# Optimization experiments

Hardware: AMD Instinct MI355X
Metric: run time of the kernel (lower is better)

The kernel has to match this reference:

```python
import jax, jax.numpy as jnp
import numpy as np

DIM = 1024
N_HEADS = 16
HEAD_DIM = DIM // N_HEADS
COND_DIM = 1024
MLP_RATIO = 4
B = 8
L = 1024  # per-sequence length (equal lengths -> T = B*L packed tokens)
T = B * L
EPS = 1e-5


def setup_inputs() -> dict:
    key = jax.random.key(0)
    ks = jax.random.split(key, 16)
    s = 0.02
    # rotary tables: [max_pos, head_dim//2]
    inv_freq = 1.0 / (10000.0 ** (jnp.arange(0, HEAD_DIM, 2, dtype=jnp.float32) / HEAD_DIM))
    t = jnp.arange(L, dtype=jnp.float32)
    freqs = t[:, None] * inv_freq[None, :]  # [L, HEAD_DIM//2]
    return {
        "x": jax.random.normal(ks[0], (T, DIM), jnp.float32),
        "lengths": jnp.full((B,), L, dtype=jnp.int64),
        "offsets": jnp.arange(B, dtype=jnp.int64) * L,
        "cos": jnp.cos(freqs),
        "sin": jnp.sin(freqs),
        "positions": jnp.tile(jnp.arange(L, dtype=jnp.int64), B),
        "c": jax.random.normal(ks[1], (B, COND_DIM), jnp.float32),
        "ln1_w": jnp.ones((DIM,), jnp.float32),
        "Wq": jax.random.normal(ks[2], (DIM, DIM), jnp.float32) * s,
        "Wk": jax.random.normal(ks[3], (DIM, DIM), jnp.float32) * s,
        "Wv": jax.random.normal(ks[4], (DIM, DIM), jnp.float32) * s,
        "Wo": jax.random.normal(ks[5], (DIM, DIM), jnp.float32) * s,
        "ln2_w": jnp.ones((DIM,), jnp.float32),
        "W1": jax.random.normal(ks[6], (DIM, MLP_RATIO * DIM), jnp.float32) * s,
        "b1": jnp.zeros((MLP_RATIO * DIM,), jnp.float32),
        "W2": jax.random.normal(ks[7], (MLP_RATIO * DIM, DIM), jnp.float32) * s,
        "b2": jnp.zeros((DIM,), jnp.float32),
        "ada_w": jax.random.normal(ks[8], (COND_DIM, 6 * DIM), jnp.float32) * s,
        "ada_b": jnp.zeros((6 * DIM,), jnp.float32),
    }


def _layer_norm(x, w):
    # LayerNorm with weight only (no bias), as in the torch module
    mu = jnp.mean(x, axis=-1, keepdims=True)
    var = jnp.mean(jnp.square(x - mu), axis=-1, keepdims=True)
    return (x - mu) * jax.lax.rsqrt(var + EPS) * w


def _rope(q, k, cos, sin, positions):
    # q, k: [T, H, D]; cos/sin: [max_pos, D//2]; half-split RoPE
    c = cos[positions][:, None, :]  # [T, 1, D//2]
    s = sin[positions][:, None, :]
    def rot(x):
        x1, x2 = jnp.split(x, 2, axis=-1)
        return jnp.concatenate([x1 * c - x2 * s, x2 * c + x1 * s], axis=-1)
    return rot(q), rot(k)


def reference(x, lengths, offsets, cos, sin, positions, c,
              ln1_w, Wq, Wk, Wv, Wo, ln2_w, W1, b1, W2, b2, ada_w, ada_b):
    # adaLN modulation: [B, 6*DIM] -> six [B, DIM]
    ada = c @ ada_w + ada_b
    sh_msa, sc_msa, g_msa, sh_mlp, sc_mlp, g_mlp = jnp.split(ada, 6, axis=-1)
    # per-token gather via seq_ids (equal lengths -> repeat each row L times)
    seq_ids = jnp.repeat(jnp.arange(B), L)  # = repeat_interleave(arange(B), lengths)
    sh_msa_t, sc_msa_t, g_msa_t = sh_msa[seq_ids], sc_msa[seq_ids], g_msa[seq_ids]
    sh_mlp_t, sc_mlp_t, g_mlp_t = sh_mlp[seq_ids], sc_mlp[seq_ids], g_mlp[seq_ids]

    x_skip = x
    h = _layer_norm(x, ln1_w) * (1.0 + sc_msa_t) + sh_msa_t
    q = (h @ Wq).reshape(T, N_HEADS, HEAD_DIM)
    k = (h @ Wk).reshape(T, N_HEADS, HEAD_DIM)
    v = (h @ Wv).reshape(T, N_HEADS, HEAD_DIM)
    q, k = _rope(q, k, cos, sin, positions)

    # intra-sequence-only attention: with equal lengths the block-diagonal
    # score_mod mask is exactly per-sequence attention -> reshape to [B, L, H, D]
    qb = q.reshape(B, L, N_HEADS, HEAD_DIM)
    kb = k.reshape(B, L, N_HEADS, HEAD_DIM)
    vb = v.reshape(B, L, N_HEADS, HEAD_DIM)
    scores = jnp.einsum('blhd,bmhd->bhlm', qb, kb) / jnp.sqrt(jnp.float32(HEAD_DIM))
    probs = jax.nn.softmax(scores, axis=-1)
    attn = jnp.einsum('bhlm,bmhd->blhd', probs, vb).reshape(T, DIM)

    x = x_skip + g_msa_t * (attn @ Wo)  # dropout p is identity in eval mode

    h2 = _layer_norm(x, ln2_w) * (1.0 + sc_mlp_t) + sh_mlp_t
    mlp = jax.nn.gelu(h2 @ W1 + b1, approximate=True) @ W2 + b2
    return x + g_mlp_t * mlp
```

## Files before the change

kernel.cpp:

```cpp
#include <hip/hip_runtime.h>

typedef unsigned short u16;
typedef __attribute__((ext_vector_type(8))) short short8;
typedef __attribute__((ext_vector_type(4))) float f32x4;
typedef __attribute__((ext_vector_type(4))) unsigned uint4v;

__device__ __forceinline__ float bf2f(u16 u){
  unsigned v = ((unsigned)u) << 16;
  return __builtin_bit_cast(float, v);
}
__device__ __forceinline__ u16 f2bf(float f){
  unsigned u = __builtin_bit_cast(unsigned, f);
  u += 0x7fff + ((u >> 16) & 1);
  return (u16)(u >> 16);
}
__device__ __forceinline__ unsigned packbf(float lo, float hi){
  return ((unsigned)f2bf(hi) << 16) | (unsigned)f2bf(lo);
}
__device__ __forceinline__ void async16(const void* g, void* l){
  __builtin_amdgcn_global_load_lds((const __attribute__((address_space(1))) void*)g,
                                   (__attribute__((address_space(3))) void*)l, 16, 0, 0);
}
#define VMW(n) asm volatile("s_waitcnt vmcnt(" #n ")" ::: "memory")

__global__ __launch_bounds__(256) void ada_partial(
    const float* __restrict__ c, const float* __restrict__ aw,
    float* __restrict__ part){
  int n  = blockIdx.x*256 + threadIdx.x;
  int b  = blockIdx.y;
  int kc = blockIdx.z;
  const float* cr  = c + b*1024 + kc*128;
  const float* awp = aw + (size_t)(kc*128)*6144 + n;
  float acc = 0.f;
#pragma unroll 8
  for (int k = 0; k < 128; ++k)
    acc += cr[k] * awp[(size_t)k*6144];
  part[(size_t)(kc*8 + b)*6144 + n] = acc;
}

__global__ __launch_bounds__(256) void ada_reduce(
    const float* __restrict__ part, const float* __restrict__ ab,
    float* __restrict__ ada){
  int idx = blockIdx.x*256 + threadIdx.x;
  int n = idx % 6144;
  float acc = ab[n];
#pragma unroll
  for (int kc = 0; kc < 8; ++kc)
    acc += part[(size_t)kc*49152 + idx];
  ada[idx] = acc;
}

__global__ __launch_bounds__(256) void transpose_cast(
    const float* __restrict__ src, u16* __restrict__ dst, int K, int N){
  __shared__ float t[64][65];
  int n0 = blockIdx.x*64, k0 = blockIdx.y*64;
  int tid = threadIdx.x;
  int cc = tid & 63, r4 = tid >> 6;
#pragma unroll 4
  for (int it = 0; it < 16; ++it){
    int r = it*4 + r4;
    t[r][cc] = src[(size_t)(k0 + r)*N + n0 + cc];
  }
  __syncthreads();
#pragma unroll 4
  for (int it = 0; it < 16; ++it){
    int r = it*4 + r4;
    dst[(size_t)(n0 + r)*K + k0 + cc] = f2bf(t[cc][r]);
  }
}

__global__ __launch_bounds__(256) void ln_mod(
    const float* __restrict__ x, u16* __restrict__ out,
    const float* __restrict__ w, const float* __restrict__ ada,
    int shift_off, int scale_off){
  int t = blockIdx.x, tid = threadIdx.x;
  const float* xr = x + (size_t)t*1024;
  float v[4]; float s = 0.f, ss = 0.f;
#pragma unroll
  for (int i = 0; i < 4; ++i){ v[i] = xr[tid + i*256]; s += v[i]; ss += v[i]*v[i]; }
  for (int d = 1; d < 64; d <<= 1){ s += __shfl_xor(s, d); ss += __shfl_xor(ss, d); }
  __shared__ float red[8];
  int wv = tid >> 6;
  if ((tid & 63) == 0){ red[wv] = s; red[4+wv] = ss; }
  __syncthreads();
  s = red[0]+red[1]+red[2]+red[3];
  ss = red[4]+red[5]+red[6]+red[7];
  float mu = s * (1.f/1024.f);
  float var = ss * (1.f/1024.f) - mu*mu;
  float rs = rsqrtf(var + 1e-5f);
  int b = t >> 10;
  const float* sh = ada + b*6144 + shift_off;
  const float* sc = ada + b*6144 + scale_off;
#pragma unroll
  for (int i = 0; i < 4; ++i){
    int cidx = tid + i*256;
    float hh = (v[i]-mu)*rs*w[cidx]*(1.f + sc[cidx]) + sh[cidx];
    out[(size_t)t*1024 + cidx] = f2bf(hh);
  }
}

template<int EPI>
__device__ __forceinline__ void gemm_epi(
    void* Cout, int m, int n, int N, int m_off, float v,
    const float* e0, const float* e1, const float* e2){
  if (EPI == 0){
    ((u16*)Cout)[(size_t)m*N + n] = f2bf(v);
  } else if (EPI == 1){
    const int b = (m + m_off) >> 10;
    float g = e1[b*6144 + 2048 + n];
    ((float*)Cout)[(size_t)m*N + n] = e0[(size_t)m*N + n] + g*v;
  } else if (EPI == 2){
    float xx = v + e0[n];
    float u = xx*(1.5957691216f + 0.07135481626f*xx*xx);
    ((u16*)Cout)[(size_t)m*N + n] = f2bf(xx / (1.f + __expf(-u)));
  } else {
    const int b = (m + m_off) >> 10;
    float g = e1[b*6144 + 5120 + n];
    ((float*)Cout)[(size_t)m*N + n] = e2[(size_t)m*N + n] + g*(v + e0[n]);
  }
}

__device__ __forceinline__ void xcd_remap(int& bx, int& by){
  const int nx = gridDim.x;
  const int yb = gridDim.y >> 3;
  const int bid = blockIdx.y*nx + blockIdx.x;
  const int g = bid & 7, ii = bid >> 3;
  bx = ii % nx;
  by = g*yb + ii/nx;
}

template<int EPI>
__global__ __launch_bounds__(512, 2) void gemm_bt(
    const u16* __restrict__ A, const u16* __restrict__ Bt,
    void* __restrict__ Cout, int M, int N, int K, int m_off,
    const float* __restrict__ e0, const float* __restrict__ e1,
    const float* __restrict__ e2){
  __shared__ u16 lds[32768];
  const int tid = threadIdx.x;
  const int wv = tid >> 6, lane = tid & 63;
  const int quad = lane >> 4, ln = lane & 15;
  const int wr = wv >> 2, wc = wv & 3;
  int bx, by; xcd_remap(bx, by);
  const int n0 = bx*256, m0 = by*256;
  const int nt = K >> 5;

  const int swslot = (lane & 3) ^ ((lane >> 3) & 3);
  const u16* Ap = A  + (size_t)(m0 + wv*16 + (lane>>2))*K + swslot*8;
  const u16* Bp = Bt + (size_t)(n0 + wv*16 + (lane>>2))*K + swslot*8;
  const size_t hstep = (size_t)128*K;
  u16* lw = lds + wv*512;

  f32x4 acc[8][4] = {};

  async16(Ap,         lw);
  async16(Ap + hstep, lw + 4096);
  async16(Bp,         lw + 8192);
  async16(Bp + hstep, lw + 12288);
  VMW(0);
  __builtin_amdgcn_s_barrier();

  const int rsw = (quad ^ ((ln >> 1) & 3))*8;
  const u16* Ar = lds + (wr*128 + ln)*32 + rsw;
  const u16* Br = lds + 8192 + (wc*64 + ln)*32 + rsw;

  for (int t = 0; t < nt; ++t){
    const int bo = (t & 1)*16384;
    short8 bfr[4], af[4];
#pragma unroll
    for (int j = 0; j < 4; ++j) bfr[j] = *(const short8*)(Br + bo + j*512);
#pragma unroll
    for (int i = 0; i < 4; ++i) af[i]  = *(const short8*)(Ar + bo + i*512);
    if (t + 1 < nt){
      u16* d = lw + ((t+1)&1)*16384;
      async16(Ap + (size_t)(t+1)*32,         d);
      async16(Ap + hstep + (size_t)(t+1)*32, d + 4096);
      async16(Bp + (size_t)(t+1)*32,         d + 8192);
      async16(Bp + hstep + (size_t)(t+1)*32, d + 12288);
    }
    __builtin_amdgcn_s_setprio(1);
#pragma unroll
    for (int i = 0; i < 4; ++i)
#pragma unroll
      for (int j = 0; j < 4; ++j)
        acc[i][j] = __builtin_amdgcn_mfma_f32_16x16x32_bf16(af[i], bfr[j], acc[i][j], 0, 0, 0);
#pragma unroll
    for (int i = 0; i < 4; ++i) af[i] = *(const short8*)(Ar + bo + 2048 + i*512);
#pragma unroll
    for (int i = 0; i < 4; ++i)
#pragma unroll
      for (int j = 0; j < 4; ++j)
        acc[4+i][j] = __builtin_amdgcn_mfma_f32_16x16x32_bf16(af[i], bfr[j], acc[4+i][j], 0, 0, 0);
    __builtin_amdgcn_s_setprio(0);
    VMW(0);
    __builtin_amdgcn_s_barrier();
  }

  const int mB = m0 + wr*128 + quad*4;
  const int nB = n0 + wc*64 + ln;
#pragma unroll
  for (int i = 0; i < 8; ++i)
#pragma unroll
    for (int r = 0; r < 4; ++r)
#pragma unroll
      for (int j = 0; j < 4; ++j)
        gemm_epi<EPI>(Cout, mB + i*16 + r, nB + j*16, N, m_off, acc[i][j][r], e0, e1, e2);
}

template<int EPI>
__global__ __launch_bounds__(256, 4) void gemm_bt128(
    const u16* __restrict__ A, const u16* __restrict__ Bt,
    void* __restrict__ Cout, int M, int N, int K, int m_off,
    const float* __restrict__ e0, const float* __restrict__ e1,
    const float* __restrict__ e2){
  __shared__ u16 lds[32768];
  const int tid = threadIdx.x;
  const int wv = tid >> 6, lane = tid & 63;
  const int quad = lane >> 4, ln = lane & 15;
  const int wr = wv >> 1, wc = wv & 1;
  int bx, by; xcd_remap(bx, by);
  const int n0 = bx*128, m0 = by*128;
  const int nt = K >> 5;

  const int swslot = (lane & 3) ^ ((lane >> 3) & 3);
  const u16* Ap = A  + (size_t)(m0 + wv*16 + (lane>>2))*K + swslot*8;
  const u16* Bp = Bt + (size_t)(n0 + wv*16 + (lane>>2))*K + swslot*8;
  const size_t hstep = (size_t)64*K;
  u16* lw = lds + wv*512;

  f32x4 acc[4][4] = {};

#pragma unroll
  for (int tau = 0; tau < 3; ++tau){
    u16* d = lw + tau*8192;
    async16(Ap + (size_t)tau*32,         d);
    async16(Ap + hstep + (size_t)tau*32, d + 2048);
    async16(Bp + (size_t)tau*32,         d + 4096);
    async16(Bp + hstep + (size_t)tau*32, d + 6144);
  }
  VMW(8);
  __builtin_amdgcn_s_barrier();

  const int rsw = (quad ^ ((ln >> 1) & 3))*8;
  const u16* Ar = lds + (wr*64 + ln)*32 + rsw;
  const u16* Br = lds + 4096 + (wc*64 + ln)*32 + rsw;

  for (int t = 0; t < nt; ++t){
    const int bo = (t & 3)*8192;
    short8 bfr[4], af[2];
#pragma unroll
    for (int j = 0; j < 4; ++j) bfr[j] = *(const short8*)(Br + bo + j*512);
#pragma unroll
    for (int i = 0; i < 2; ++i) af[i]  = *(const short8*)(Ar + bo + i*512);
    if (t + 3 < nt){
      u16* d = lw + ((t+3)&3)*8192;
      async16(Ap + (size_t)(t+3)*32,         d);
      async16(Ap + hstep + (size_t)(t+3)*32, d + 2048);
      async16(Bp + (size_t)(t+3)*32,         d + 4096);
      async16(Bp + hstep + (size_t)(t+3)*32, d + 6144);
    }
    __builtin_amdgcn_s_setprio(1);
#pragma unroll
    for (int i = 0; i < 2; ++i)
#pragma unroll
      for (int j = 0; j < 4; ++j)
        acc[i][j] = __builtin_amdgcn_mfma_f32_16x16x32_bf16(af[i], bfr[j], acc[i][j], 0, 0, 0);
#pragma unroll
    for (int i = 0; i < 2; ++i) af[i] = *(const short8*)(Ar + bo + 1024 + i*512);
#pragma unroll
    for (int i = 0; i < 2; ++i)
#pragma unroll
      for (int j = 0; j < 4; ++j)
        acc[2+i][j] = __builtin_amdgcn_mfma_f32_16x16x32_bf16(af[i], bfr[j], acc[2+i][j], 0, 0, 0);
    __builtin_amdgcn_s_setprio(0);
    if (t + 4 <= nt)      VMW(8);
    else if (t + 3 == nt) VMW(4);
    else if (t + 2 == nt) VMW(0);
    __builtin_amdgcn_s_barrier();
  }

  const int mB = m0 + wr*64 + quad*4;
  const int nB = n0 + wc*64 + ln;
#pragma unroll
  for (int i = 0; i < 4; ++i)
#pragma unroll
    for (int r = 0; r < 4; ++r)
#pragma unroll
      for (int j = 0; j < 4; ++j)
        gemm_epi<EPI>(Cout, mB + i*16 + r, nB + j*16, N, m_off, acc[i][j][r], e0, e1, e2);
}

__global__ __launch_bounds__(256) void rope_pack(
    const u16* __restrict__ qkv, const float* __restrict__ cosT,
    const float* __restrict__ sinT, u16* __restrict__ qp,
    u16* __restrict__ kp, u16* __restrict__ vt){
  int blk = blockIdx.x;
  int lt = blk & 15, h = (blk >> 4) & 15, b = blk >> 8;
  int l0 = lt*64;
  int bh = b*16 + h;
  __shared__ u16 vl[64][68];
  int tid = threadIdx.x;
  size_t tile_base = (size_t)bh*65536 + (size_t)lt*4096;
#pragma unroll 4
  for (int it = 0; it < 16; ++it){
    int idx = it*256 + tid;
    int r = idx >> 6, d = idx & 63;
    int t = b*1024 + l0 + r;
    int pos = l0 + r;
    const u16* row = qkv + (size_t)t*3072 + h*64;
    float qv = bf2f(row[d]), kv = bf2f(row[1024+d]);
    float qo, ko;
    if (d < 32){
      float cs = cosT[pos*32 + d], sn = sinT[pos*32 + d];
      qo = qv*cs - bf2f(row[d+32])*sn;
      ko = kv*cs - bf2f(row[1024+d+32])*sn;
    } else {
      int dd = d - 32;
      float cs = cosT[pos*32 + dd], sn = sinT[pos*32 + dd];
      qo = qv*cs + bf2f(row[d-32])*sn;
      ko = kv*cs + bf2f(row[1024+d-32])*sn;
    }
    qp[((size_t)bh*1024 + l0 + r)*64 + d] = f2bf(qo*0.125f);
    int ksl = ((d&31) >> 3) ^ ((r >> 1) & 3);
    kp[tile_base + (d>>5)*2048 + r*32 + (ksl<<3) + (d&7)] = f2bf(ko);
    vl[d][r] = row[2048 + d];
  }
  __syncthreads();
#pragma unroll 4
  for (int it = 0; it < 16; ++it){
    int idx = it*256 + tid;
    int d = idx >> 6, cc = idx & 63;
    int vsl = ((cc&31) >> 3) ^ ((d >> 1) & 3);
    vt[tile_base + (cc>>5)*2048 + d*32 + (vsl<<3) + (cc&7)] = vl[d][cc];
  }
}

__global__ __launch_bounds__(256) void attn_kernel(
    const u16* __restrict__ qp, const u16* __restrict__ kp,
    const u16* __restrict__ vtp, u16* __restrict__ ao){
  __shared__ u16 Kb[2][4096];
  __shared__ u16 Vb[2][4096];
  int tid = threadIdx.x, w = tid >> 6, lane = tid & 63;
  int quad = lane >> 4, ln = lane & 15;
  int bh = blockIdx.x & 127, qb = blockIdx.x >> 7;
  int h = bh & 15, b = bh >> 4;
  const u16* Q  = qp  + ((size_t)bh*1024 + qb*64 + w*16)*64;
  const u16* Kg = kp  + (size_t)bh*65536 + lane*8;
  const u16* Vg = vtp + (size_t)bh*65536 + lane*8;
  short8 qf0 = *(const short8*)(Q + ln*64 + quad*8);
  short8 qf1 = *(const short8*)(Q + ln*64 + 32 + quad*8);
  f32x4 o[4] = {};
  float m = -3e38f, l = 0.f;
  const int rsw = (quad ^ ((ln >> 1) & 3))*8;

  async16(Kg + (w*2+0)*512, Kb[0] + (w*2+0)*512);
  async16(Kg + (w*2+1)*512, Kb[0] + (w*2+1)*512);
  async16(Vg + (w*2+0)*512, Vb[0] + (w*2+0)*512);
  async16(Vg + (w*2+1)*512, Vb[0] + (w*2+1)*512);

  for (int kt = 0; kt < 16; ++kt){
    const int cur = kt & 1;
    if (kt < 15){
      const u16* ktg = Kg + (kt+1)*4096;
      const u16* vtg = Vg + (kt+1)*4096;
      async16(ktg + (w*2+0)*512, Kb[cur^1] + (w*2+0)*512);
      async16(ktg + (w*2+1)*512, Kb[cur^1] + (w*2+1)*512);
      async16(vtg + (w*2+0)*512, Vb[cur^1] + (w*2+0)*512);
      async16(vtg + (w*2+1)*512, Vb[cur^1] + (w*2+1)*512);
      VMW(4);
    } else {
      VMW(0);
    }
    __builtin_amdgcn_s_barrier();
    f32x4 zz = {0.f, 0.f, 0.f, 0.f};
    f32x4 st[4];
    __builtin_amdgcn_s_setprio(1);
#pragma unroll
    for (int c = 0; c < 4; ++c){
      short8 k0 = *(const short8*)(Kb[cur] +        (c*16 + ln)*32 + rsw);
      short8 k1 = *(const short8*)(Kb[cur] + 2048 + (c*16 + ln)*32 + rsw);
      st[c] = __builtin_amdgcn_mfma_f32_16x16x32_bf16(k0, qf0, zz, 0,0,0);
      st[c] = __builtin_amdgcn_mfma_f32_16x16x32_bf16(k1, qf1, st[c], 0,0,0);
    }
    __builtin_amdgcn_s_setprio(0);
    short8 va[4][2];
#pragma unroll
    for (int dc = 0; dc < 4; ++dc)
#pragma unroll
      for (int kh = 0; kh < 2; ++kh)
        va[dc][kh] = *(const short8*)(Vb[cur] + kh*2048 + (dc*16 + ln)*32 + rsw);
    float mx = st[0][0];
#pragma unroll
    for (int c = 0; c < 4; ++c)
#pragma unroll
      for (int r = 0; r < 4; ++r) mx = fmaxf(mx, st[c][r]);
    mx = fmaxf(mx, __shfl_xor(mx, 16));
    mx = fmaxf(mx, __shfl_xor(mx, 32));
    if (__any(mx > m + 8.f)){
      float mn = fmaxf(m, mx);
      float alpha = __expf(m - mn);
      m = mn;
      l *= alpha;
#pragma unroll
      for (int dc = 0; dc < 4; ++dc)
#pragma unroll
        for (int r = 0; r < 4; ++r) o[dc][r] *= alpha;
    }
    float p[4][4];
#pragma unroll
    for (int c = 0; c < 4; ++c)
#pragma unroll
      for (int r = 0; r < 4; ++r) p[c][r] = __expf(st[c][r] - m);
    float sum = ((p[0][0]+p[0][1]) + (p[0][2]+p[0][3])) + ((p[1][0]+p[1][1]) + (p[1][2]+p[1][3]))
              + ((p[2][0]+p[2][1]) + (p[2][2]+p[2][3])) + ((p[3][0]+p[3][1]) + (p[3][2]+p[3][3]));
    sum += __shfl_xor(sum, 16);
    sum += __shfl_xor(sum, 32);
    l += sum;
    unsigned pc[4][2];
#pragma unroll
    for (int c = 0; c < 4; ++c){
      pc[c][0] = packbf(p[c][0], p[c][1]);
      pc[c][1] = packbf(p[c][2], p[c][3]);
    }
    const int sA = ((quad & 1)*2)*16 + ln;
    const int sB = sA + 16;
    const bool hi = quad >= 2;
#pragma unroll
    for (int kh = 0; kh < 2; ++kh){
      unsigned a0 = (unsigned)__shfl((int)pc[2*kh][0],   sA);
      unsigned b0 = (unsigned)__shfl((int)pc[2*kh+1][0], sA);
      unsigned a1 = (unsigned)__shfl((int)pc[2*kh][1],   sA);
      unsigned b1 = (unsigned)__shfl((int)pc[2*kh+1][1], sA);
      unsigned a2 = (unsigned)__shfl((int)pc[2*kh][0],   sB);
      unsigned b2 = (unsigned)__shfl((int)pc[2*kh+1][0], sB);
      unsigned a3 = (unsigned)__shfl((int)pc[2*kh][1],   sB);
      unsigned b3 = (unsigned)__shfl((int)pc[2*kh+1][1], sB);
      uint4v u = { hi ? b0 : a0, hi ? b1 : a1, hi ? b2 : a2, hi ? b3 : a3 };
      short8 pfrag = __builtin_bit_cast(short8, u);
      __builtin_amdgcn_s_setprio(1);
#pragma unroll
      for (int dc = 0; dc < 4; ++dc)
        o[dc] = __builtin_amdgcn_mfma_f32_16x16x32_bf16(va[dc][kh], pfrag, o[dc], 0,0,0);
      __builtin_amdgcn_s_setprio(0);
    }
    __builtin_amdgcn_s_barrier();
  }
  float rl = 1.f / l;
  size_t orow = ((size_t)b*1024 + qb*64 + w*16 + ln)*1024 + h*64;
#pragma unroll
  for (int dc = 0; dc < 4; ++dc)
#pragma unroll
    for (int r = 0; r < 4; ++r)
      ao[orow + dc*16 + quad*4 + r] = f2bf(o[dc][r] * rl);
}

extern "C" void kernel_launch(void* const* d_in, const int* in_sizes, int n_in,
                              void* d_out, int out_size, void* d_ws, size_t ws_size,
                              hipStream_t stream){
  const float* x    = (const float*)d_in[0];
  const float* cosT = (const float*)d_in[3];
  const float* sinT = (const float*)d_in[4];
  const float* c    = (const float*)d_in[6];
  const float* ln1w = (const float*)d_in[7];
  const float* Wq   = (const float*)d_in[8];
  const float* Wk   = (const float*)d_in[9];
  const float* Wv   = (const float*)d_in[10];
  const float* Wo   = (const float*)d_in[11];
  const float* ln2w = (const float*)d_in[12];
  const float* W1   = (const float*)d_in[13];
  const float* b1   = (const float*)d_in[14];
  const float* W2   = (const float*)d_in[15];
  const float* b2   = (const float*)d_in[16];
  const float* adaW = (const float*)d_in[17];
  const float* adaB = (const float*)d_in[18];

  char* ws = (char*)d_ws;
  float* ada  = (float*)(ws);
  u16* wqkvt  = (u16*)  (ws + 262144);
  u16* wot    = (u16*)  (ws + 6553600);
  u16* w1t    = (u16*)  (ws + 8650752);
  u16* w2t    = (u16*)  (ws + 17039360);
  u16* h      = (u16*)  (ws + 25427968);
  u16* qp     = (u16*)  (ws + 25427968);
  u16* h2     = (u16*)  (ws + 25427968);
  u16* qkv    = (u16*)  (ws + 42205184);
  u16* attnb  = (u16*)  (ws + 42205184);
  float* xmid = (float*)(ws + 58982400);
  float* adaP = (float*)(ws + 92536832);
  u16* kp     = (u16*)  (ws + 92536832);
  u16* vt     = (u16*)  (ws + 109314048);
  u16* hid    = (u16*)  (ws + 92536832);
  u16* hidF   = (u16*)  (ws + 126091264);
  float* out  = (float*)d_out;
  const bool bigws = ws_size >= (size_t)193200128;

  ada_partial<<<dim3(24,8,8), 256, 0, stream>>>(c, adaW, adaP);
  ada_reduce<<<192, 256, 0, stream>>>(adaP, adaB, ada);
  transpose_cast<<<dim3(16,16), 256, 0, stream>>>(Wq, wqkvt,             1024, 1024);
  transpose_cast<<<dim3(16,16), 256, 0, stream>>>(Wk, wqkvt + 1024*1024, 1024, 1024);
  transpose_cast<<<dim3(16,16), 256, 0, stream>>>(Wv, wqkvt + 2048*1024, 1024, 1024);
  transpose_cast<<<dim3(16,16), 256, 0, stream>>>(Wo, wot,               1024, 1024);
  transpose_cast<<<dim3(64,16), 256, 0, stream>>>(W1, w1t,               1024, 4096);
  transpose_cast<<<dim3(16,64), 256, 0, stream>>>(W2, w2t,               4096, 1024);
  ln_mod<<<8192, 256, 0, stream>>>(x, h, ln1w, ada, 0, 1024);
  gemm_bt128<0><<<dim3(24,64), 256, 0, stream>>>(h, wqkvt, qkv, 8192, 3072, 1024, 0,
                                                 nullptr, nullptr, nullptr);
  rope_pack<<<2048, 256, 0, stream>>>(qkv, cosT, sinT, qp, kp, vt);
  attn_kernel<<<2048, 256, 0, stream>>>(qp, kp, vt, attnb);
  gemm_bt128<1><<<dim3(8,64), 256, 0, stream>>>(attnb, wot, xmid, 8192, 1024, 1024, 0,
                                                x, ada, nullptr);
  ln_mod<<<8192, 256, 0, stream>>>(xmid, h2, ln2w, ada, 3072, 4096);
  if (bigws){
    gemm_bt<2><<<dim3(16,32), 512, 0, stream>>>(h2, w1t, hidF, 8192, 4096, 1024, 0,
                                                b1, nullptr, nullptr);
    gemm_bt128<3><<<dim3(8,64), 256, 0, stream>>>(hidF, w2t, out, 8192, 1024, 4096, 0,
                                                  b2, ada, xmid);
  } else {
    for (int cch = 0; cch < 2; ++cch){
      const size_t mo = (size_t)cch*4096;
      gemm_bt<2><<<dim3(16,16), 512, 0, stream>>>(h2 + mo*1024, w1t, hid,
                                                  4096, 4096, 1024, (int)mo,
                                                  b1, nullptr, nullptr);
      gemm_bt128<3><<<dim3(8,32), 256, 0, stream>>>(hid, w2t, out + mo*1024,
                                                    4096, 1024, 4096, (int)mo,
                                                    b2, ada, xmid + mo*1024);
    }
  }
}
```

Before: 581.8 us.

## Restructure 256x256 GEMM into 8-phase K=64 double-buffered pipeline

The 256x256 bf16 GEMM moves from a K=32 double-buffered loop to K=64 tiles in a 128KB LDS double buffer, with a new 8-way XOR swizzle. Each iteration handles two tiles in eight phases that interleave LDS fragment reads, partial async global-to-LDS loads and 16-MFMA bursts, separated by barriers and staged vmcnt waits. The goal is to hide global load latency behind MFMA work and cut per-K-step overhead. In exchange it uses twice the LDS per block, which likely allows only one 512-thread block per CU despite the launch bounds of 2, and it adds many barriers.

Result: slower. 608.8 us (+4.6%).

```diff
diff --git a/kernel.cpp b/kernel.cpp
--- a/kernel.cpp
+++ b/kernel.cpp
@@ -22,6 +22,7 @@
                                    (__attribute__((address_space(3))) void*)l, 16, 0, 0);
 }
 #define VMW(n) asm volatile("s_waitcnt vmcnt(" #n ")" ::: "memory")
+#define BARR() __builtin_amdgcn_s_barrier()
 
 __global__ __launch_bounds__(256) void ada_partial(
     const float* __restrict__ c, const float* __restrict__ aw,
@@ -129,71 +130,149 @@
   by = g*yb + ii/nx;
 }
 
+__device__ __forceinline__ void mfma16(f32x4 (&acc)[8][4], const short8 (&af)[4],
+                                       const short8 (&bf)[4], int ro){
+#pragma unroll
+  for (int i = 0; i < 4; ++i)
+#pragma unroll
+    for (int j = 0; j < 4; ++j)
+      acc[ro+i][j] = __builtin_amdgcn_mfma_f32_16x16x32_bf16(af[i], bf[j], acc[ro+i][j], 0,0,0);
+}
+__device__ __forceinline__ void ld4(short8 (&f)[4], const u16* base){
+#pragma unroll
+  for (int i = 0; i < 4; ++i) f[i] = *(const short8*)(base + i*1024);
+}
+
 template<int EPI>
 __global__ __launch_bounds__(512, 2) void gemm_bt(
     const u16* __restrict__ A, const u16* __restrict__ Bt,
     void* __restrict__ Cout, int M, int N, int K, int m_off,
     const float* __restrict__ e0, const float* __restrict__ e1,
     const float* __restrict__ e2){
-  __shared__ u16 lds[32768];
+  __shared__ u16 lds[65536];
   const int tid = threadIdx.x;
   const int wv = tid >> 6, lane = tid & 63;
   const int quad = lane >> 4, ln = lane & 15;
   const int wr = wv >> 2, wc = wv & 3;
   int bx, by; xcd_remap(bx, by);
   const int n0 = bx*256, m0 = by*256;
-  const int nt = K >> 5;
-
-  const int swslot = (lane & 3) ^ ((lane >> 3) & 3);
-  const u16* Ap = A  + (size_t)(m0 + wv*16 + (lane>>2))*K + swslot*8;
-  const u16* Bp = Bt + (size_t)(n0 + wv*16 + (lane>>2))*K + swslot*8;
-  const size_t hstep = (size_t)128*K;
-  u16* lw = lds + wv*512;
+  const int nIt = K >> 7;
+
+  const int srow  = wv*8 + (lane>>3);
+  const int sslot = (lane&7) ^ ((lane>>3)&7);
+  const u16* ApS = A  + (size_t)(m0 + srow)*K + sslot*8;
+  const u16* BpS = Bt + (size_t)(n0 + srow)*K + sslot*8;
+  const size_t qstep = (size_t)64*K;
+
+#define STA(s, T, buf) async16(ApS + (size_t)(s)*qstep + (size_t)(T)*64, \
+                               lds + (buf)*32768 + (s)*4096 + wv*512 + lane*8)
+#define STB(s, T, buf) async16(BpS + (size_t)(s)*qstep + (size_t)(T)*64, \
+                               lds + (buf)*32768 + 16384 + (s)*4096 + wv*512 + lane*8)
 
   f32x4 acc[8][4] = {};
-
-  async16(Ap,         lw);
-  async16(Ap + hstep, lw + 4096);
-  async16(Bp,         lw + 8192);
-  async16(Bp + hstep, lw + 12288);
-  VMW(0);
-  __builtin_amdgcn_s_barrier();
-
-  const int rsw = (quad ^ ((ln >> 1) & 3))*8;
-  const u16* Ar = lds + (wr*128 + ln)*32 + rsw;
-  const u16* Br = lds + 8192 + (wc*64 + ln)*32 + rsw;
-
-  for (int t = 0; t < nt; ++t){
-    const int bo = (t & 1)*16384;
-    short8 bfr[4], af[4];
-#pragma unroll
-    for (int j = 0; j < 4; ++j) bfr[j] = *(const short8*)(Br + bo + j*512);
-#pragma unroll
-    for (int i = 0; i < 4; ++i) af[i]  = *(const short8*)(Ar + bo + i*512);
-    if (t + 1 < nt){
-      u16* d = lw + ((t+1)&1)*16384;
-      async16(Ap + (size_t)(t+1)*32,         d);
-      async16(Ap + hstep + (size_t)(t+1)*32, d + 4096);
-      async16(Bp + (size_t)(t+1)*32,         d + 8192);
-      async16(Bp + hstep + (size_t)(t+1)*32, d + 12288);
-    }
-    __builtin_amdgcn_s_setprio(1);
-#pragma unroll
-    for (int i = 0; i < 4; ++i)
-#pragma unroll
-      for (int j = 0; j < 4; ++j)
-        acc[i][j] = __builtin_amdgcn_mfma_f32_16x16x32_bf16(af[i], bfr[j], acc[i][j], 0, 0, 0);
-#pragma unroll
-    for (int i = 0; i < 4; ++i) af[i] = *(const short8*)(Ar + bo + 2048 + i*512);
-#pragma unroll
-    for (int i = 0; i < 4; ++i)
-#pragma unroll
-      for (int j = 0; j < 4; ++j)
-        acc[4+i][j] = __builtin_amdgcn_mfma_f32_16x16x32_bf16(af[i], bfr[j], acc[4+i][j], 0, 0, 0);
-    __builtin_amdgcn_s_setprio(0);
+  short8 af[4], bfr0[4], bfr1[4];
+
+  const int aBase = (wr*128 + ln)*64;
+  const int bBase = 16384 + (wc*64 + ln)*64;
+  const int sw0 = (( quad    ) ^ (ln&7))*8;
+  const int sw1 = ((4 + quad ) ^ (ln&7))*8;
+
+  STB(0,0,0); STB(1,0,0); STB(2,0,0); STB(3,0,0);
+  STA(0,0,0); STA(2,0,0); STA(1,0,0); STA(3,0,0);
+  VMW(2);
+  BARR();
+
+  for (int it = 0; it < nIt - 1; ++it){
+    const int T1 = 2*it + 1, T2 = 2*it + 2;
+    ld4(af, lds + aBase + sw0); ld4(bfr0, lds + bBase + sw0);
+    STB(0,T1,1); STB(1,T1,1);
+    BARR();
+    __builtin_amdgcn_s_setprio(1); mfma16(acc, af, bfr0, 0); __builtin_amdgcn_s_setprio(0);
+    BARR();
+    ld4(af, lds + aBase + sw1); ld4(bfr1, lds + bBase + sw1);
+    STB(2,T1,1); STB(3,T1,1);
+    BARR();
+    __builtin_amdgcn_s_setprio(1); mfma16(acc, af, bfr1, 0); __builtin_amdgcn_s_setprio(0);
+    VMW(4);
+    BARR();
+    ld4(af, lds + aBase + 4096 + sw0);
+    STA(0,T1,1); STA(2,T1,1);
+    BARR();
+    __builtin_amdgcn_s_setprio(1); mfma16(acc, af, bfr0, 4); __builtin_amdgcn_s_setprio(0);
+    BARR();
+    ld4(af, lds + aBase + 4096 + sw1);
+    STA(1,T1,1); STA(3,T1,1);
+    BARR();
+    __builtin_amdgcn_s_setprio(1); mfma16(acc, af, bfr1, 4); __builtin_amdgcn_s_setprio(0);
+    VMW(2);
+    BARR();
+    ld4(af, lds + 32768 + aBase + sw0); ld4(bfr0, lds + 32768 + bBase + sw0);
+    STB(0,T2,0); STB(1,T2,0);
+    BARR();
+    __builtin_amdgcn_s_setprio(1); mfma16(acc, af, bfr0, 0); __builtin_amdgcn_s_setprio(0);
+    BARR();
+    ld4(af, lds + 32768 + aBase + sw1); ld4(bfr1, lds + 32768 + bBase + sw1);
+    STB(2,T2,0); STB(3,T2,0);
+    BARR();
+    __builtin_amdgcn_s_setprio(1); mfma16(acc, af, bfr1, 0); __builtin_amdgcn_s_setprio(0);
+    VMW(4);
+    BARR();
+    ld4(af, lds + 32768 + aBase + 4096 + sw0);
+    STA(0,T2,0); STA(2,T2,0);
+    BARR();
+    __builtin_amdgcn_s_setprio(1); mfma16(acc, af, bfr0, 4); __builtin_amdgcn_s_setprio(0);
+    BARR();
+    ld4(af, lds + 32768 + aBase + 4096 + sw1);
+    STA(1,T2,0); STA(3,T2,0);
+    BARR();
+    __builtin_amdgcn_s_setprio(1); mfma16(acc, af, bfr1, 4); __builtin_amdgcn_s_setprio(0);
+    VMW(2);
+    BARR();
+  }
+  {
+    const int T1 = 2*nIt - 1;
+    ld4(af, lds + aBase + sw0); ld4(bfr0, lds + bBase + sw0);
+    STB(0,T1,1); STB(1,T1,1);
+    BARR();
+    __builtin_amdgcn_s_setprio(1); mfma16(acc, af, bfr0, 0); __builtin_amdgcn_s_setprio(0);
+    BARR();
+    ld4(af, lds + aBase + sw1); ld4(bfr1, lds + bBase + sw1);
+    STB(2,T1,1); STB(3,T1,1);
+    BARR();
+    __builtin_amdgcn_s_setprio(1); mfma16(acc, af, bfr1, 0); __builtin_amdgcn_s_setprio(0);
+    VMW(4);
+    BARR();
+    ld4(af, lds + aBase + 4096 + sw0);
+    STA(0,T1,1); STA(2,T1,1);
+    BARR();
+    __builtin_amdgcn_s_setprio(1); mfma16(acc, af, bfr0, 4); __builtin_amdgcn_s_setprio(0);
+    BARR();
+    ld4(af, lds + aBase + 4096 + sw1);
+    STA(1,T1,1); STA(3,T1,1);
+    BARR();
+    __builtin_amdgcn_s_setprio(1); mfma16(acc, af, bfr1, 4); __builtin_amdgcn_s_setprio(0);
+    VMW(2);
+    BARR();
+    ld4(af, lds + 32768 + aBase + sw0); ld4(bfr0, lds + 32768 + bBase + sw0);
+    BARR();
+    __builtin_amdgcn_s_setprio(1); mfma16(acc, af, bfr0, 0); __builtin_amdgcn_s_setprio(0);
+    BARR();
+    ld4(af, lds + 32768 + aBase + sw1); ld4(bfr1, lds + 32768 + bBase + sw1);
+    BARR();
+    __builtin_amdgcn_s_setprio(1); mfma16(acc, af, bfr1, 0); __builtin_amdgcn_s_setprio(0);
     VMW(0);
-    __builtin_amdgcn_s_barrier();
-  }
+    BARR();
+    ld4(af, lds + 32768 + aBase + 4096 + sw0);
+    BARR();
+    __builtin_amdgcn_s_setprio(1); mfma16(acc, af, bfr0, 4); __builtin_amdgcn_s_setprio(0);
+    BARR();
+    ld4(af, lds + 32768 + aBase + 4096 + sw1);
+    BARR();
+    __builtin_amdgcn_s_setprio(1); mfma16(acc, af, bfr1, 4); __builtin_amdgcn_s_setprio(0);
+    BARR();
+  }
+#undef STA
+#undef STB
 
   const int mB = m0 + wr*128 + quad*4;
   const int nB = n0 + wc*64 + ln;
@@ -238,7 +317,7 @@
     async16(Bp + hstep + (size_t)tau*32, d + 6144);
   }
   VMW(8);
-  __builtin_amdgcn_s_barrier();
+  BARR();
 
   const int rsw = (quad ^ ((ln >> 1) & 3))*8;
   const u16* Ar = lds + (wr*64 + ln)*32 + rsw;
@@ -275,7 +354,7 @@
     if (t + 4 <= nt)      VMW(8);
     else if (t + 3 == nt) VMW(4);
     else if (t + 2 == nt) VMW(0);
-    __builtin_amdgcn_s_barrier();
+    BARR();
   }
 
   const int mB = m0 + wr*64 + quad*4;
@@ -370,7 +449,7 @@
     } else {
       VMW(0);
     }
-    __builtin_amdgcn_s_barrier();
+    BARR();
     f32x4 zz = {0.f, 0.f, 0.f, 0.f};
     f32x4 st[4];
     __builtin_amdgcn_s_setprio(1);
@@ -442,7 +521,7 @@
         o[dc] = __builtin_amdgcn_mfma_f32_16x16x32_bf16(va[dc][kh], pfrag, o[dc], 0,0,0);
       __builtin_amdgcn_s_setprio(0);
     }
-    __builtin_amdgcn_s_barrier();
+    BARR();
   }
   float rl = 1.f / l;
   size_t orow = ((size_t)b*1024 + qb*64 + w*16 + ln)*1024 + h*64;
```
